# Kernel optimization log

Hardware: AMD Instinct MI355X
Metric: run time of the kernel (lower is better)

Reference implementation:

```python
import jax, jax.numpy as jnp
import numpy as np

L, B, S, D, W = 3, 32, 512, 512, 3
EPS = 1e-6

def setup_inputs() -> dict:
    key = jax.random.key(0)
    ks = jax.random.split(key, 12)
    s = 1.0 / np.sqrt(D)
    def n(k, shape, scale=1.0):
        return jax.random.normal(k, shape, dtype=jnp.float32) * scale
    return {
        'x': n(ks[0], (B, S, D)),
        'fwd_pad': n(ks[1], (L, W, D), s),
        'bwd_pad': n(ks[2], (L, W, D), s),
        'fwd_w': n(ks[3], (L, W + 1)),
        'bwd_w': n(ks[4], (L, W + 1)),
        'fwd_w1': n(ks[5], (L, D, D), s),
        'fwd_b1': jnp.zeros((L, D), jnp.float32),
        'fwd_w2': n(ks[6], (L, D, D), s),
        'fwd_b2': jnp.zeros((L, D), jnp.float32),
        'fwd_g': jnp.ones((L, D), jnp.float32),
        'fwd_beta': jnp.zeros((L, D), jnp.float32),
        'bwd_w1': n(ks[7], (L, D, D), s),
        'bwd_b1': jnp.zeros((L, D), jnp.float32),
        'bwd_w2': n(ks[8], (L, D, D), s),
        'bwd_b2': jnp.zeros((L, D), jnp.float32),
        'bwd_g': jnp.ones((L, D), jnp.float32),
        'bwd_beta': jnp.zeros((L, D), jnp.float32),
    }

def _ln(y, g, b):
    # Annotated-transformer LayerNorm: a2*(x-mean)/(std+eps)+b2, unbiased std
    m = y.mean(-1, keepdims=True)
    sd = jnp.std(y, -1, keepdims=True, ddof=1)
    return g * (y - m) / (sd + EPS) + b

def _ffn(y, w1, b1, w2, b2):
    h = jax.nn.relu(jnp.einsum('bsd,de->bse', y, w1) + b1)
    return jnp.einsum('bse,ef->bsf', h, w2) + b2

def _wsum(padded, w, seq_len, offset):
    # weighted sum over a sliding window of width W+1 (dropout=0, eval mode)
    win = jnp.stack([padded[:, offset + k: offset + k + seq_len] for k in range(W + 1)], 0)
    return jnp.einsum('k,kbsd->bsd', w, win)

def reference(x, fwd_pad, bwd_pad, fwd_w, bwd_w,
              fwd_w1, fwd_b1, fwd_w2, fwd_b2, fwd_g, fwd_beta,
              bwd_w1, bwd_b1, bwd_w2, bwd_b2, bwd_g, bwd_beta):
    bsz, seq_len, _ = x.shape
    xf, xb = x, x
    outs = []
    for i in range(L):
        fp = jnp.broadcast_to(fwd_pad[i], (bsz, W, D))
        bp = jnp.broadcast_to(bwd_pad[i], (bsz, W, D))
        pf = jnp.concatenate([fp, xf, bp], axis=1)  # [B, S+2W, D]
        pb = jnp.concatenate([fp, xb, bp], axis=1)
        yf = _wsum(pf, fwd_w[i], seq_len, 0)       # windows [t, t+W]
        yb = _wsum(pb, bwd_w[i], seq_len, W)       # windows [t+W, t+2W]
        xf = yf + _ffn(_ln(yf, fwd_g[i], fwd_beta[i]), fwd_w1[i], fwd_b1[i], fwd_w2[i], fwd_b2[i])
        xb = yb + _ffn(_ln(yb, bwd_g[i], bwd_beta[i]), bwd_w1[i], bwd_b1[i], bwd_w2[i], bwd_b2[i])
        outs.append(jnp.concatenate([xf, xb], axis=-1))
    return jnp.stack(outs, 0)  # [L, B, S, 2D]
```

## Files before the change

### kernel.cpp

```cpp
#include <hip/hip_runtime.h>

#define S_LEN 512
#define D_DIM 512
#define BATCH 32
#define M_ROWS (BATCH * S_LEN)
#define NLAYER 3

typedef unsigned short ushort_t;
typedef __bf16 bf16_t;
typedef bf16_t bf16x8 __attribute__((ext_vector_type(8)));
typedef unsigned short u16x8 __attribute__((ext_vector_type(8)));
typedef float f32x4 __attribute__((ext_vector_type(4)));

typedef const __attribute__((address_space(1))) unsigned int* gptr_t;
typedef __attribute__((address_space(3))) unsigned int* lptr_t;

__device__ __forceinline__ ushort_t f2bf(float f) {
  unsigned u = __float_as_uint(f);
  unsigned r = (u + 0x7fffu + ((u >> 16) & 1u)) >> 16;
  return (ushort_t)r;
}

__global__ __launch_bounds__(256)
void wprep_kernel(const float* __restrict__ fw1, const float* __restrict__ fw2,
                  const float* __restrict__ bw1, const float* __restrict__ bw2,
                  ushort_t* __restrict__ wt1, ushort_t* __restrict__ wt2) {
  int z = blockIdx.z;
  int l = z >> 2, m = z & 3;
  const float* bases[4] = {fw1, fw2, bw1, bw2};
  const float* src = bases[m] + (size_t)l * D_DIM * D_DIM;
  int streamIdx = m >> 1;
  int which = m & 1;
  ushort_t* dst = (which ? wt2 : wt1) + ((size_t)streamIdx * NLAYER + l) * D_DIM * D_DIM;

  __shared__ float tile[32][33];
  int n0 = blockIdx.x * 32, k0 = blockIdx.y * 32;
  int tx = threadIdx.x, ty = threadIdx.y;
#pragma unroll
  for (int i = 0; i < 32; i += 8)
    tile[ty + i][tx] = src[(size_t)(k0 + ty + i) * D_DIM + n0 + tx];
  __syncthreads();
#pragma unroll
  for (int i = 0; i < 32; i += 8)
    dst[(size_t)(n0 + ty + i) * D_DIM + k0 + tx] = f2bf(tile[tx][ty + i]);
}

__global__ __launch_bounds__(256)
void conv_ln_kernel(const float* __restrict__ srcF, int strideF,
                    const float* __restrict__ srcB, int strideB,
                    const float* __restrict__ padLo, const float* __restrict__ padHi,
                    const float* __restrict__ wF, const float* __restrict__ wB,
                    const float* __restrict__ gF, const float* __restrict__ beF,
                    const float* __restrict__ gB, const float* __restrict__ beB,
                    float* __restrict__ yf, ushort_t* __restrict__ yln) {
  int z = blockIdx.y;
  int tid = threadIdx.x;
  int lane = tid & 63;
  int rl = tid >> 6;
  int row = blockIdx.x * 4 + rl;
  int t = row & (S_LEN - 1);
  const float* src = z ? srcB : srcF;
  int stride = z ? strideB : strideF;
  const float* wv = z ? wB : wF;
  const float* gv = z ? gB : gF;
  const float* bv = z ? beB : beF;
  int toff = z ? 0 : -3;
  int c0 = lane * 4, c1 = 256 + lane * 4;

  float4 a0 = make_float4(0.f, 0.f, 0.f, 0.f);
  float4 a1 = make_float4(0.f, 0.f, 0.f, 0.f);
#pragma unroll
  for (int k = 0; k < 4; ++k) {
    int tt = t + k + toff;
    const float* rp;
    if (tt < 0)            rp = padLo + (size_t)(tt + 3) * D_DIM;
    else if (tt >= S_LEN)  rp = padHi + (size_t)(tt - S_LEN) * D_DIM;
    else                   rp = src + (size_t)(row + k + toff) * stride;
    float wk = wv[k];
    float4 u0 = *(const float4*)(rp + c0);
    float4 u1 = *(const float4*)(rp + c1);
    a0.x = fmaf(wk, u0.x, a0.x); a0.y = fmaf(wk, u0.y, a0.y);
    a0.z = fmaf(wk, u0.z, a0.z); a0.w = fmaf(wk, u0.w, a0.w);
    a1.x = fmaf(wk, u1.x, a1.x); a1.y = fmaf(wk, u1.y, a1.y);
    a1.z = fmaf(wk, u1.z, a1.z); a1.w = fmaf(wk, u1.w, a1.w);
  }
  float s = a0.x + a0.y + a0.z + a0.w + a1.x + a1.y + a1.z + a1.w;
#pragma unroll
  for (int o = 32; o; o >>= 1) s += __shfl_xor(s, o);
  float mean = s * (1.0f / 512.0f);
  float q = 0.f, dx;
  dx = a0.x - mean; q = fmaf(dx, dx, q);
  dx = a0.y - mean; q = fmaf(dx, dx, q);
  dx = a0.z - mean; q = fmaf(dx, dx, q);
  dx = a0.w - mean; q = fmaf(dx, dx, q);
  dx = a1.x - mean; q = fmaf(dx, dx, q);
  dx = a1.y - mean; q = fmaf(dx, dx, q);
  dx = a1.z - mean; q = fmaf(dx, dx, q);
  dx = a1.w - mean; q = fmaf(dx, dx, q);
#pragma unroll
  for (int o = 32; o; o >>= 1) q += __shfl_xor(q, o);
  float sd = sqrtf(q * (1.0f / 511.0f));
  float inv = 1.0f / (sd + 1e-6f);

  size_t base = ((size_t)z * M_ROWS + row) * D_DIM;
  *(float4*)(yf + base + c0) = a0;
  *(float4*)(yf + base + c1) = a1;

  float4 g0 = *(const float4*)(gv + c0), g1 = *(const float4*)(gv + c1);
  float4 b0 = *(const float4*)(bv + c0), b1 = *(const float4*)(bv + c1);
  ushort_t p0[4], p1[4];
  p0[0] = f2bf(g0.x * ((a0.x - mean) * inv) + b0.x);
  p0[1] = f2bf(g0.y * ((a0.y - mean) * inv) + b0.y);
  p0[2] = f2bf(g0.z * ((a0.z - mean) * inv) + b0.z);
  p0[3] = f2bf(g0.w * ((a0.w - mean) * inv) + b0.w);
  p1[0] = f2bf(g1.x * ((a1.x - mean) * inv) + b1.x);
  p1[1] = f2bf(g1.y * ((a1.y - mean) * inv) + b1.y);
  p1[2] = f2bf(g1.z * ((a1.z - mean) * inv) + b1.z);
  p1[3] = f2bf(g1.w * ((a1.w - mean) * inv) + b1.w);
  *(uint2*)(yln + base + c0) = *(uint2*)p0;
  *(uint2*)(yln + base + c1) = *(uint2*)p1;
}

template <int EPI>
__global__ __launch_bounds__(256)
void gemm_kernel(const ushort_t* __restrict__ A,
                 const ushort_t* __restrict__ Bt_f, const ushort_t* __restrict__ Bt_b,
                 const float* __restrict__ bias_f, const float* __restrict__ bias_b,
                 const float* __restrict__ resid,
                 ushort_t* __restrict__ Hout,
                 float* __restrict__ Cout) {
  const int K = 512;
  int mblk = blockIdx.x;
  int nblk = blockIdx.y;
  int z = blockIdx.z;
  const ushort_t* Ab = A + (size_t)z * M_ROWS * K + (size_t)mblk * 128 * K;
  const ushort_t* Bb = (z ? Bt_b : Bt_f) + (size_t)nblk * 128 * K;

  __shared__ __attribute__((aligned(16))) ushort_t As[128 * 32];
  __shared__ __attribute__((aligned(16))) ushort_t Bs[128 * 32];

  int tid = threadIdx.x, lane = tid & 63, wave = tid >> 6;
  int wr = wave >> 1, wc = wave & 1;
  int lm = lane & 15, lq = lane >> 4;

  f32x4 acc[4][4] = {};

  for (int kb = 0; kb < 16; ++kb) {
    int k0 = kb * 32;
#pragma unroll
    for (int i = 0; i < 2; ++i) {
      int slot = i * 256 + tid;
      int row = slot >> 2, kc = slot & 3;
      const ushort_t* ga = Ab + (size_t)row * K + k0 + kc * 8;
      const ushort_t* gb = Bb + (size_t)row * K + k0 + kc * 8;
      __builtin_amdgcn_global_load_lds((gptr_t)(const void*)ga,
                                       (lptr_t)(void*)(As + slot * 8), 16, 0, 0);
      __builtin_amdgcn_global_load_lds((gptr_t)(const void*)gb,
                                       (lptr_t)(void*)(Bs + slot * 8), 16, 0, 0);
    }
    __syncthreads();
    bf16x8 a[4], b[4];
#pragma unroll
    for (int i = 0; i < 4; ++i) {
      union { u16x8 u; bf16x8 b; } ua, ub;
      ua.u = *(const u16x8*)&As[(wr * 64 + i * 16 + lm) * 32 + lq * 8];
      ub.u = *(const u16x8*)&Bs[(wc * 64 + i * 16 + lm) * 32 + lq * 8];
      a[i] = ua.b; b[i] = ub.b;
    }
#pragma unroll
    for (int i = 0; i < 4; ++i)
#pragma unroll
      for (int j = 0; j < 4; ++j)
        acc[i][j] = __builtin_amdgcn_mfma_f32_16x16x32_bf16(a[i], b[j], acc[i][j], 0, 0, 0);
    __syncthreads();
  }

  const float* bias = z ? bias_b : bias_f;
  if (EPI == 1) {
    ushort_t* Hb = Hout + (size_t)z * M_ROWS * 512;
#pragma unroll
    for (int i = 0; i < 4; ++i) {
      int mbase = mblk * 128 + wr * 64 + i * 16 + lq * 4;
#pragma unroll
      for (int j = 0; j < 4; ++j) {
        int n = nblk * 128 + wc * 64 + j * 16 + lm;
        float bvn = bias[n];
#pragma unroll
        for (int r = 0; r < 4; ++r) {
          float v = fmaxf(acc[i][j][r] + bvn, 0.0f);
          Hb[(size_t)(mbase + r) * 512 + n] = f2bf(v);
        }
      }
    }
  } else {
    const float* rs = resid + (size_t)z * M_ROWS * 512;
    float* Cb = Cout + (size_t)z * 512;
#pragma unroll
    for (int i = 0; i < 4; ++i) {
      int mbase = mblk * 128 + wr * 64 + i * 16 + lq * 4;
#pragma unroll
      for (int j = 0; j < 4; ++j) {
        int n = nblk * 128 + wc * 64 + j * 16 + lm;
        float bvn = bias[n];
#pragma unroll
        for (int r = 0; r < 4; ++r) {
          float v = acc[i][j][r] + bvn + rs[(size_t)(mbase + r) * 512 + n];
          Cb[(size_t)(mbase + r) * 1024 + n] = v;
        }
      }
    }
  }
}

extern "C" void kernel_launch(void* const* d_in, const int* in_sizes, int n_in,
                              void* d_out, int out_size, void* d_ws, size_t ws_size,
                              hipStream_t stream) {
  const float* x        = (const float*)d_in[0];
  const float* fwd_pad  = (const float*)d_in[1];
  const float* bwd_pad  = (const float*)d_in[2];
  const float* fwd_w    = (const float*)d_in[3];
  const float* bwd_w    = (const float*)d_in[4];
  const float* fwd_w1   = (const float*)d_in[5];
  const float* fwd_b1   = (const float*)d_in[6];
  const float* fwd_w2   = (const float*)d_in[7];
  const float* fwd_b2   = (const float*)d_in[8];
  const float* fwd_g    = (const float*)d_in[9];
  const float* fwd_beta = (const float*)d_in[10];
  const float* bwd_w1   = (const float*)d_in[11];
  const float* bwd_b1   = (const float*)d_in[12];
  const float* bwd_w2   = (const float*)d_in[13];
  const float* bwd_b2   = (const float*)d_in[14];
  const float* bwd_g    = (const float*)d_in[15];
  const float* bwd_beta = (const float*)d_in[16];
  float* out = (float*)d_out;

  const size_t WSZ = (size_t)D_DIM * D_DIM;
  ushort_t* wt1 = (ushort_t*)d_ws;
  ushort_t* wt2 = wt1 + 2 * NLAYER * WSZ;
  float* yf = (float*)(wt2 + 2 * NLAYER * WSZ);
  ushort_t* yln = (ushort_t*)(yf + (size_t)2 * M_ROWS * D_DIM);
  ushort_t* h = yln + (size_t)2 * M_ROWS * D_DIM;

  wprep_kernel<<<dim3(16, 16, 12), dim3(32, 8), 0, stream>>>(
      fwd_w1, fwd_w2, bwd_w1, bwd_w2, wt1, wt2);

  for (int l = 0; l < NLAYER; ++l) {
    const float *srcF, *srcB;
    int strF, strB;
    if (l == 0) {
      srcF = x; srcB = x; strF = 512; strB = 512;
    } else {
      srcF = out + (size_t)(l - 1) * M_ROWS * 1024;
      srcB = srcF + 512;
      strF = 1024; strB = 1024;
    }
    conv_ln_kernel<<<dim3(M_ROWS / 4, 2), 256, 0, stream>>>(
        srcF, strF, srcB, strB,
        fwd_pad + (size_t)l * 3 * D_DIM, bwd_pad + (size_t)l * 3 * D_DIM,
        fwd_w + l * 4, bwd_w + l * 4,
        fwd_g + l * D_DIM, fwd_beta + l * D_DIM,
        bwd_g + l * D_DIM, bwd_beta + l * D_DIM,
        yf, yln);

    gemm_kernel<1><<<dim3(128, 4, 2), 256, 0, stream>>>(
        yln, wt1 + (size_t)l * WSZ, wt1 + (size_t)(NLAYER + l) * WSZ,
        fwd_b1 + l * D_DIM, bwd_b1 + l * D_DIM,
        nullptr, h, nullptr);

    gemm_kernel<2><<<dim3(128, 4, 2), 256, 0, stream>>>(
        h, wt2 + (size_t)l * WSZ, wt2 + (size_t)(NLAYER + l) * WSZ,
        fwd_b2 + l * D_DIM, bwd_b2 + l * D_DIM,
        yf, nullptr, out + (size_t)l * M_ROWS * 1024);
  }
}
```

Baseline: 557.0 us.

## Recompute window sum in GEMM2 epilogue and remap blocks for XCD locality

Stops conv_ln from writing the fp32 window-sum tensor yf. The second GEMM epilogue now recomputes the residual from the source activations, pads and window weights, loading 7 rows per 4 outputs. The GEMM grid is also flattened to 1D and remapped so each XCD handles a contiguous range of M-blocks sharing the same A rows across the 4 N-blocks, aiming for better L2 reuse. This trades a 32MB fp32 write plus read per layer for extra scattered reads in the epilogue.

```diff
diff --git a/kernel.cpp b/kernel.cpp
--- a/kernel.cpp
+++ b/kernel.cpp
@@ -52,7 +52,7 @@
                     const float* __restrict__ wF, const float* __restrict__ wB,
                     const float* __restrict__ gF, const float* __restrict__ beF,
                     const float* __restrict__ gB, const float* __restrict__ beB,
-                    float* __restrict__ yf, ushort_t* __restrict__ yln) {
+                    ushort_t* __restrict__ yln) {
   int z = blockIdx.y;
   int tid = threadIdx.x;
   int lane = tid & 63;
@@ -103,9 +103,6 @@
   float inv = 1.0f / (sd + 1e-6f);
 
   size_t base = ((size_t)z * M_ROWS + row) * D_DIM;
-  *(float4*)(yf + base + c0) = a0;
-  *(float4*)(yf + base + c1) = a1;
-
   float4 g0 = *(const float4*)(gv + c0), g1 = *(const float4*)(gv + c1);
   float4 b0 = *(const float4*)(bv + c0), b1 = *(const float4*)(bv + c1);
   ushort_t p0[4], p1[4];
@@ -126,13 +123,21 @@
 void gemm_kernel(const ushort_t* __restrict__ A,
                  const ushort_t* __restrict__ Bt_f, const ushort_t* __restrict__ Bt_b,
                  const float* __restrict__ bias_f, const float* __restrict__ bias_b,
-                 const float* __restrict__ resid,
                  ushort_t* __restrict__ Hout,
-                 float* __restrict__ Cout) {
+                 float* __restrict__ Cout,
+                 const float* __restrict__ srcF, const float* __restrict__ srcB,
+                 int srcStride,
+                 const float* __restrict__ padLo, const float* __restrict__ padHi,
+                 const float* __restrict__ wF, const float* __restrict__ wB) {
   const int K = 512;
-  int mblk = blockIdx.x;
-  int nblk = blockIdx.y;
-  int z = blockIdx.z;
+  int lin = blockIdx.x;
+  int xcd = lin & 7;
+  int slot = lin >> 3;
+  int nblk = slot & 3;
+  int G = xcd * 32 + (slot >> 2);
+  int z = G >> 7;
+  int mblk = G & 127;
+
   const ushort_t* Ab = A + (size_t)z * M_ROWS * K + (size_t)mblk * 128 * K;
   const ushort_t* Bb = (z ? Bt_b : Bt_f) + (size_t)nblk * 128 * K;
 
@@ -149,14 +154,14 @@
     int k0 = kb * 32;
 #pragma unroll
     for (int i = 0; i < 2; ++i) {
-      int slot = i * 256 + tid;
-      int row = slot >> 2, kc = slot & 3;
+      int slot2 = i * 256 + tid;
+      int row = slot2 >> 2, kc = slot2 & 3;
       const ushort_t* ga = Ab + (size_t)row * K + k0 + kc * 8;
       const ushort_t* gb = Bb + (size_t)row * K + k0 + kc * 8;
       __builtin_amdgcn_global_load_lds((gptr_t)(const void*)ga,
-                                       (lptr_t)(void*)(As + slot * 8), 16, 0, 0);
+                                       (lptr_t)(void*)(As + slot2 * 8), 16, 0, 0);
       __builtin_amdgcn_global_load_lds((gptr_t)(const void*)gb,
-                                       (lptr_t)(void*)(Bs + slot * 8), 16, 0, 0);
+                                       (lptr_t)(void*)(Bs + slot2 * 8), 16, 0, 0);
     }
     __syncthreads();
     bf16x8 a[4], b[4];
@@ -193,19 +198,35 @@
       }
     }
   } else {
-    const float* rs = resid + (size_t)z * M_ROWS * 512;
+    const float* src = z ? srcB : srcF;
+    const float* wv = z ? wB : wF;
+    int toff = z ? 0 : -3;
+    float w0 = wv[0], w1 = wv[1], w2 = wv[2], w3 = wv[3];
     float* Cb = Cout + (size_t)z * 512;
 #pragma unroll
     for (int i = 0; i < 4; ++i) {
       int mbase = mblk * 128 + wr * 64 + i * 16 + lq * 4;
+      int t0 = mbase & (S_LEN - 1);
+      int rb = mbase - t0;
+      const float* rp[7];
+#pragma unroll
+      for (int q = 0; q < 7; ++q) {
+        int tt = t0 + toff + q;
+        rp[q] = (tt < 0)       ? padLo + (size_t)(tt + 3) * D_DIM
+              : (tt >= S_LEN)  ? padHi + (size_t)(tt - S_LEN) * D_DIM
+                               : src + (size_t)(rb + tt) * srcStride;
+      }
 #pragma unroll
       for (int j = 0; j < 4; ++j) {
         int n = nblk * 128 + wc * 64 + j * 16 + lm;
+        float v[7];
+#pragma unroll
+        for (int q = 0; q < 7; ++q) v[q] = rp[q][n];
         float bvn = bias[n];
 #pragma unroll
         for (int r = 0; r < 4; ++r) {
-          float v = acc[i][j][r] + bvn + rs[(size_t)(mbase + r) * 512 + n];
-          Cb[(size_t)(mbase + r) * 1024 + n] = v;
+          float y = w0 * v[r] + w1 * v[r + 1] + w2 * v[r + 2] + w3 * v[r + 3];
+          Cb[(size_t)(mbase + r) * 1024 + n] = acc[i][j][r] + bvn + y;
         }
       }
     }
@@ -237,39 +258,43 @@
   const size_t WSZ = (size_t)D_DIM * D_DIM;
   ushort_t* wt1 = (ushort_t*)d_ws;
   ushort_t* wt2 = wt1 + 2 * NLAYER * WSZ;
-  float* yf = (float*)(wt2 + 2 * NLAYER * WSZ);
-  ushort_t* yln = (ushort_t*)(yf + (size_t)2 * M_ROWS * D_DIM);
-  ushort_t* h = yln + (size_t)2 * M_ROWS * D_DIM;
+  ushort_t* yln = wt2 + 2 * NLAYER * WSZ;
+  ushort_t* h   = yln + (size_t)2 * M_ROWS * D_DIM;
 
   wprep_kernel<<<dim3(16, 16, 12), dim3(32, 8), 0, stream>>>(
       fwd_w1, fwd_w2, bwd_w1, bwd_w2, wt1, wt2);
 
   for (int l = 0; l < NLAYER; ++l) {
     const float *srcF, *srcB;
-    int strF, strB;
+    int str;
     if (l == 0) {
-      srcF = x; srcB = x; strF = 512; strB = 512;
+      srcF = x; srcB = x; str = 512;
     } else {
       srcF = out + (size_t)(l - 1) * M_ROWS * 1024;
       srcB = srcF + 512;
-      strF = 1024; strB = 1024;
-    }
+      str = 1024;
+    }
+    const float* pLo = fwd_pad + (size_t)l * 3 * D_DIM;
+    const float* pHi = bwd_pad + (size_t)l * 3 * D_DIM;
+
     conv_ln_kernel<<<dim3(M_ROWS / 4, 2), 256, 0, stream>>>(
-        srcF, strF, srcB, strB,
-        fwd_pad + (size_t)l * 3 * D_DIM, bwd_pad + (size_t)l * 3 * D_DIM,
+        srcF, str, srcB, str, pLo, pHi,
         fwd_w + l * 4, bwd_w + l * 4,
         fwd_g + l * D_DIM, fwd_beta + l * D_DIM,
         bwd_g + l * D_DIM, bwd_beta + l * D_DIM,
-        yf, yln);
-
-    gemm_kernel<1><<<dim3(128, 4, 2), 256, 0, stream>>>(
+        yln);
+
+    gemm_kernel<1><<<1024, 256, 0, stream>>>(
         yln, wt1 + (size_t)l * WSZ, wt1 + (size_t)(NLAYER + l) * WSZ,
         fwd_b1 + l * D_DIM, bwd_b1 + l * D_DIM,
-        nullptr, h, nullptr);
-
-    gemm_kernel<2><<<dim3(128, 4, 2), 256, 0, stream>>>(
+        h, nullptr,
+        nullptr, nullptr, 0, nullptr, nullptr, nullptr, nullptr);
+
+    gemm_kernel<2><<<1024, 256, 0, stream>>>(
         h, wt2 + (size_t)l * WSZ, wt2 + (size_t)(NLAYER + l) * WSZ,
         fwd_b2 + l * D_DIM, bwd_b2 + l * D_DIM,
-        yf, nullptr, out + (size_t)l * M_ROWS * 1024);
+        nullptr, out + (size_t)l * M_ROWS * 1024,
+        srcF, srcB, str, pLo, pHi,
+        fwd_w + l * 4, bwd_w + l * 4);
   }
 }
```

Measured after the change: 513.4 us. 1.08x faster.
